# Kernel optimization log

Hardware: AMD Instinct MI355X
Metric: run time of the kernel (lower is better)

The kernel has to match this reference:

```python
import math
import jax, jax.numpy as jnp
import numpy as np

EMBED, HEADS, LEVELS, POINTS = 256, 8, 4, 4
HEAD_DIM = EMBED // HEADS
SHAPES = ((100, 100), (50, 50), (25, 25), (13, 13))  # (h, w) per level
BS, NQ = 8, 900
NV = sum(h * w for h, w in SHAPES)


def _offset_bias():
    # Faithful to init_weights(): per-head rotated grid init for sampling_offsets bias.
    th = np.arange(HEADS, dtype=np.float32) * (2.0 * math.pi / HEADS)
    g = np.stack([np.cos(th), np.sin(th)], -1)
    g = g / np.abs(g).max(-1, keepdims=True)
    g = np.tile(g[:, None, None, :], (1, LEVELS, POINTS, 1))
    g = g * (np.arange(POINTS, dtype=np.float32) + 1.0)[None, None, :, None]
    return jnp.asarray(g.reshape(-1))


def setup_inputs() -> dict:
    key = jax.random.key(0)
    ks = jax.random.split(key, 10)
    s = 0.05
    return {
        "query": jax.random.normal(ks[0], (BS, NQ, EMBED), jnp.float32),
        "value": jax.random.normal(ks[1], (BS, NV, EMBED), jnp.float32),
        "reference_points": jax.random.uniform(ks[2], (BS, NQ, LEVELS, 2), jnp.float32),
        "spatial_shapes": jnp.array(SHAPES, jnp.int32),
        "W_off": jax.random.normal(ks[3], (EMBED, HEADS * LEVELS * POINTS * 2), jnp.float32) * s,
        "b_off": _offset_bias(),
        "W_attn": jax.random.normal(ks[4], (EMBED, HEADS * LEVELS * POINTS), jnp.float32) * s,
        "b_attn": jnp.zeros((HEADS * LEVELS * POINTS,), jnp.float32),
        "W_v": jax.random.normal(ks[5], (EMBED, EMBED), jnp.float32) * s,
        "b_v": jnp.zeros((EMBED,), jnp.float32),
        "W_out": jax.random.normal(ks[6], (EMBED, EMBED), jnp.float32) * s,
        "b_out": jnp.zeros((EMBED,), jnp.float32),
    }


def _bilinear_sample(vl, loc, H, W, aw):
    """grid_sample bilinear, align_corners=False, zero padding, fused with attn weights.

    vl:  (bs, heads, H*W, d)   loc: (bs, nq, heads, P, 2) in [0,1] (x, y)
    aw:  (bs, heads, nq, P)    ->   (bs, heads, nq, d)
    """
    x = loc[..., 0] * W - 0.5
    y = loc[..., 1] * H - 0.5
    x0 = jnp.floor(x)
    y0 = jnp.floor(y)
    lx = x - x0
    ly = y - y0
    x0i = x0.astype(jnp.int32)
    y0i = y0.astype(jnp.int32)
    bs, heads = vl.shape[0], vl.shape[1]
    nq, P = loc.shape[1], loc.shape[3]
    acc = jnp.zeros((bs, heads, nq, vl.shape[-1]), vl.dtype)
    corners = ((0, 0, (1 - lx) * (1 - ly)), (1, 0, lx * (1 - ly)),
               (0, 1, (1 - lx) * ly), (1, 1, lx * ly))
    for dx, dy, wgt in corners:
        xi = x0i + dx
        yi = y0i + dy
        valid = ((xi >= 0) & (xi < W) & (yi >= 0) & (yi < H)).astype(vl.dtype)
        idx = jnp.clip(yi, 0, H - 1) * W + jnp.clip(xi, 0, W - 1)  # (bs, nq, heads, P)
        idx = idx.transpose(0, 2, 1, 3).reshape(bs, heads, nq * P)
        g = jnp.take_along_axis(vl, idx[..., None], axis=2).reshape(bs, heads, nq, P, -1)
        cw = (wgt * valid).transpose(0, 2, 1, 3) * aw  # (bs, heads, nq, P)
        acc = acc + (g * cw[..., None]).sum(3)
    return acc


def reference(query, value, reference_points, spatial_shapes,
              W_off, b_off, W_attn, b_attn, W_v, b_v, W_out, b_out):
    identity = query
    bs, nq, _ = query.shape
    v = (value @ W_v + b_v).reshape(bs, -1, HEADS, HEAD_DIM)
    off = (query @ W_off + b_off).reshape(bs, nq, HEADS, LEVELS, POINTS, 2)
    aw = (query @ W_attn + b_attn).reshape(bs, nq, HEADS, LEVELS * POINTS)
    aw = jax.nn.softmax(aw, -1).reshape(bs, nq, HEADS, LEVELS, POINTS)
    # offset normalizer is (w, h) per level
    norm = jnp.stack([spatial_shapes[:, 1], spatial_shapes[:, 0]], -1).astype(query.dtype)
    loc = reference_points[:, :, None, :, None, :] + off / norm[None, None, None, :, None, :]
    sizes = [h * w for h, w in SHAPES]
    starts = np.cumsum([0] + sizes[:-1])
    out = jnp.zeros((bs, HEADS, nq, HEAD_DIM), query.dtype)
    for l, (h, w) in enumerate(SHAPES):
        vl = jax.lax.dynamic_slice_in_dim(v, int(starts[l]), sizes[l], axis=1)
        vl = vl.transpose(0, 2, 1, 3)  # (bs, heads, h*w, d)
        aw_l = aw[:, :, :, l].transpose(0, 2, 1, 3)  # (bs, heads, nq, P)
        out = out + _bilinear_sample(vl, loc[:, :, :, l], h, w, aw_l)
    out = out.transpose(0, 2, 1, 3).reshape(bs, nq, EMBED)
    return out @ W_out + b_out + identity
```

## Files before the change

### kernel.cpp

```cpp
#include <hip/hip_runtime.h>
#include <hip/hip_bf16.h>

#define EMBED    256
#define HEADS    8
#define LEVELS   4
#define POINTS   4
#define HEAD_DIM 32
#define BS       8
#define NQ       900
#define NV       13294
#define MV       (BS*NV)
#define MQ       (BS*NQ)
#define NQOUT    384

typedef float  f32x4  __attribute__((ext_vector_type(4)));
typedef __bf16 bf16x8 __attribute__((ext_vector_type(8)));
typedef unsigned short ushort8  __attribute__((ext_vector_type(8)));
typedef unsigned short ushort4v __attribute__((ext_vector_type(4)));

__device__ __forceinline__ unsigned short f2bf(float f) {
    unsigned u = __builtin_bit_cast(unsigned, f);
    u += 0x7FFFu + ((u >> 16) & 1u);
    return (unsigned short)(u >> 16);
}
__device__ __forceinline__ float bf2f(unsigned short h) {
    unsigned u = ((unsigned)h) << 16;
    return __builtin_bit_cast(float, u);
}

__global__ __launch_bounds__(256) void prep_kernel(
    const float* __restrict__ Wv,  const float* __restrict__ Woff,
    const float* __restrict__ Wattn, const float* __restrict__ Wout,
    const float* __restrict__ boff, const float* __restrict__ battn,
    unsigned short* __restrict__ WtV, unsigned short* __restrict__ WtQ,
    unsigned short* __restrict__ WtO, float* __restrict__ biasQ)
{
    int n = blockIdx.x;
    int k = threadIdx.x;
    if (n < 256) {
        WtV[n * 256 + k] = f2bf(Wv [k * 256 + n]);
        WtO[n * 256 + k] = f2bf(Wout[k * 256 + n]);
        WtQ[n * 256 + k] = f2bf(Woff[k * 256 + n]);
    } else {
        int j = n - 256;
        WtQ[n * 256 + k] = f2bf(Wattn[k * 128 + j]);
    }
    if (k == 0) biasQ[n] = (n < 256) ? boff[n] : battn[n - 256];
}

template <int WPB, bool OUT_BF16, bool ADD_ID>
struct GemmOps {
    static constexpr int N = WPB * 64;

    __device__ static void load_strip(f32x4 (&pa)[16], const float* __restrict__ A,
                                      int s, int lrow, int kq) {
        const float* ab = A + (size_t)(s * 16 + lrow) * 256 + kq * 8;
        #pragma unroll
        for (int c = 0; c < 8; ++c) {
            pa[2 * c]     = *(const f32x4*)(ab + c * 32);
            pa[2 * c + 1] = *(const f32x4*)(ab + c * 32 + 4);
        }
    }

    __device__ static void compute_store(const f32x4 (&pa)[16],
                                         const bf16x8 (&wf)[4][8],
                                         const f32x4 (&bj)[4],
                                         const float* __restrict__ Ident,
                                         void* __restrict__ Cv,
                                         int s, int lrow, int kq, int n0) {
        f32x4 acc[4];
        #pragma unroll
        for (int j = 0; j < 4; ++j) acc[j] = (f32x4)0.f;
        #pragma unroll
        for (int c = 0; c < 8; ++c) {
            ushort8 vb;
            #pragma unroll
            for (int e = 0; e < 4; ++e) {
                vb[e]     = f2bf(pa[2 * c][e]);
                vb[4 + e] = f2bf(pa[2 * c + 1][e]);
            }
            bf16x8 vf = __builtin_bit_cast(bf16x8, vb);
            #pragma unroll
            for (int j = 0; j < 4; ++j)
                acc[j] = __builtin_amdgcn_mfma_f32_16x16x32_bf16(
                    wf[j][c], vf, acc[j], 0, 0, 0);
        }
        const size_t crow = (size_t)(s * 16 + lrow) * N + n0 + kq * 4;
        #pragma unroll
        for (int j = 0; j < 4; ++j) {
            f32x4 r = acc[j] + bj[j];
            if (ADD_ID)
                r += *(const f32x4*)(Ident + crow + j * 16);
            if (OUT_BF16) {
                ushort4v o;
                #pragma unroll
                for (int e = 0; e < 4; ++e) o[e] = f2bf(r[e]);
                *(ushort4v*)((unsigned short*)Cv + crow + j * 16) = o;
            } else {
                *(f32x4*)((float*)Cv + crow + j * 16) = r;
            }
        }
    }
};

template <int WPB, bool OUT_BF16, bool ADD_ID>
__global__ __launch_bounds__(WPB * 64, 1)
void gemm_regw(const float* __restrict__ A,
               const unsigned short* __restrict__ Bt,
               const float* __restrict__ bias,
               const float* __restrict__ Ident,
               void* __restrict__ Cv, int M)
{
    using Ops = GemmOps<WPB, OUT_BF16, ADD_ID>;
    const int tid  = threadIdx.x;
    const int wave = tid >> 6, lane = tid & 63;
    const int lrow = lane & 15, kq = lane >> 4;
    const int n0   = wave * 64;

    bf16x8 wf[4][8];
    #pragma unroll
    for (int j = 0; j < 4; ++j)
        #pragma unroll
        for (int c = 0; c < 8; ++c)
            wf[j][c] = *(const bf16x8*)(Bt + (size_t)(n0 + j * 16 + lrow) * 256
                                           + c * 32 + kq * 8);
    f32x4 bj[4];
    #pragma unroll
    for (int j = 0; j < 4; ++j)
        bj[j] = *(const f32x4*)(bias + n0 + j * 16 + kq * 4);

    const int NS    = M / 16;
    const int chunk = (NS + gridDim.x - 1) / gridDim.x;
    const int sbeg  = blockIdx.x * chunk;
    const int send  = min(NS, sbeg + chunk);
    if (sbeg >= send) return;

    f32x4 buf0[16], buf1[16];
    Ops::load_strip(buf0, A, sbeg, lrow, kq);
    for (int s = sbeg; s < send; s += 2) {
        if (s + 1 < send) Ops::load_strip(buf1, A, s + 1, lrow, kq);
        Ops::compute_store(buf0, wf, bj, Ident, Cv, s, lrow, kq, n0);
        if (s + 1 < send) {
            if (s + 2 < send) Ops::load_strip(buf0, A, s + 2, lrow, kq);
            Ops::compute_store(buf1, wf, bj, Ident, Cv, s + 1, lrow, kq, n0);
        }
    }
}

__device__ const int   LVL_W[4]  = {100, 50, 25, 13};
__device__ const int   LVL_H[4]  = {100, 50, 25, 13};
__device__ const int   LVL_S[4]  = {0, 10000, 12500, 13125};

__global__ __launch_bounds__(256) void sample_kernel(
    const unsigned short* __restrict__ V,
    const float* __restrict__ Qout,
    const float* __restrict__ RP,
    float* __restrict__ OutS)
{
    const int gid = blockIdx.x * 16 + (threadIdx.x >> 4);
    const int s   = threadIdx.x & 15;
    const int h   = gid & 7;
    const int bq  = gid >> 3;
    const int b   = bq / NQ;

    const float* qrow = Qout + (size_t)bq * NQOUT;

    const int l = s >> 2;
    const float ox = qrow[h * 32 + 2 * s];
    const float oy = qrow[h * 32 + 2 * s + 1];
    float logit    = qrow[256 + h * 16 + s];
    const float rpx = RP[((size_t)bq * 4 + l) * 2 + 0];
    const float rpy = RP[((size_t)bq * 4 + l) * 2 + 1];
    int W = LVL_W[l], H = LVL_H[l], st = LVL_S[l];
    float x = rpx * (float)W + ox - 0.5f;
    float y = rpy * (float)H + oy - 0.5f;
    float fx = floorf(x), fy = floorf(y);
    float lx = x - fx, ly = y - fy;
    int ix = (int)fx, iy = (int)fy;

    float mx = logit;
    #pragma unroll
    for (int o = 8; o; o >>= 1) mx = fmaxf(mx, __shfl_xor(mx, o, 16));
    float e = __expf(logit - mx);
    float sum = e;
    #pragma unroll
    for (int o = 8; o; o >>= 1) sum += __shfl_xor(sum, o, 16);
    const float wgt = e / sum;

    const unsigned short* vb = V + ((size_t)b * NV) * 256 + h * 32 + 2 * s;
    float ax0 = 0.f, ay0 = 0.f, ax1 = 0.f, ay1 = 0.f;

    #pragma unroll
    for (int sp = 0; sp < 16; ++sp) {
        float ws  = __shfl(wgt, sp, 16);
        float lxs = __shfl(lx,  sp, 16);
        float lys = __shfl(ly,  sp, 16);
        int  ixs  = __shfl(ix,  sp, 16);
        int  iys  = __shfl(iy,  sp, 16);
        int  Ws   = __shfl(W,   sp, 16);
        int  Hs   = __shfl(H,   sp, 16);
        int  sts  = __shfl(st,  sp, 16);
        #pragma unroll
        for (int corner = 0; corner < 4; ++corner) {
            int dx = corner & 1, dy = corner >> 1;
            int xi = ixs + dx, yi = iys + dy;
            float valid = (xi >= 0 && xi < Ws && yi >= 0 && yi < Hs) ? 1.f : 0.f;
            int xc = min(max(xi, 0), Ws - 1);
            int yc = min(max(yi, 0), Hs - 1);
            float cw = ws * (dx ? lxs : 1.f - lxs) * (dy ? lys : 1.f - lys) * valid;
            const unsigned short* p = vb + (size_t)(sts + yc * Ws + xc) * 256;
            unsigned pv = *(const unsigned*)p;
            if (corner & 1) {
                ax1 = fmaf(cw, bf2f((unsigned short)(pv & 0xFFFF)), ax1);
                ay1 = fmaf(cw, bf2f((unsigned short)(pv >> 16)), ay1);
            } else {
                ax0 = fmaf(cw, bf2f((unsigned short)(pv & 0xFFFF)), ax0);
                ay0 = fmaf(cw, bf2f((unsigned short)(pv >> 16)), ay0);
            }
        }
    }
    float2* o = (float2*)(OutS + (size_t)bq * 256 + h * 32);
    o[s] = make_float2(ax0 + ax1, ay0 + ay1);
}

extern "C" void kernel_launch(void* const* d_in, const int* in_sizes, int n_in,
                              void* d_out, int out_size, void* d_ws, size_t ws_size,
                              hipStream_t stream)
{
    const float* query  = (const float*)d_in[0];
    const float* value  = (const float*)d_in[1];
    const float* rp     = (const float*)d_in[2];
    const float* W_off  = (const float*)d_in[4];
    const float* b_off  = (const float*)d_in[5];
    const float* W_attn = (const float*)d_in[6];
    const float* b_attn = (const float*)d_in[7];
    const float* W_v    = (const float*)d_in[8];
    const float* b_v    = (const float*)d_in[9];
    const float* W_out  = (const float*)d_in[10];
    const float* b_out  = (const float*)d_in[11];

    char* ws = (char*)d_ws;
    size_t off = 0;
    unsigned short* Vbf = (unsigned short*)(ws + off); off += (size_t)MV * 256 * 2;
    float* qout         = (float*)(ws + off);          off += (size_t)MQ * NQOUT * 4;
    float* outs         = (float*)(ws + off);          off += (size_t)MQ * 256 * 4;
    unsigned short* WtV = (unsigned short*)(ws + off); off += 256 * 256 * 2;
    unsigned short* WtQ = (unsigned short*)(ws + off); off += 384 * 256 * 2;
    unsigned short* WtO = (unsigned short*)(ws + off); off += 256 * 256 * 2;
    float* biasQ        = (float*)(ws + off);          off += 384 * 4;

    prep_kernel<<<384, 256, 0, stream>>>(W_v, W_off, W_attn, W_out, b_off, b_attn,
                                         WtV, WtQ, WtO, biasQ);

    gemm_regw<4, true, false><<<512, 256, 0, stream>>>(
        value, WtV, b_v, nullptr, Vbf, MV);

    gemm_regw<6, false, false><<<450, 384, 0, stream>>>(
        query, WtQ, biasQ, nullptr, qout, MQ);

    sample_kernel<<<(BS * NQ * HEADS) / 16, 256, 0, stream>>>(Vbf, qout, rp, outs);

    gemm_regw<4, false, true><<<450, 256, 0, stream>>>(
        outs, WtO, b_out, query, (float*)d_out, MQ);
}
```

Baseline: 317.6 us.

## Stage GEMM weights in LDS and split N across grid blocks

Replaces the register-resident-weight GEMM with a version that copies a 128-column weight slice into padded shared memory and reads MFMA B fragments from LDS. The N dimension is split across blockIdx.y, and two waves per column set take alternating row strips, with A loaded in half-K pieces to overlap loads with compute. This is meant to lower register pressure so more waves fit per CU, at the cost of extra LDS reads, re-reading A once per N slice, and launch_bounds no longer capping occupancy at 1.

Result: faster. 285.3 us (-10.2%).

```diff
diff --git a/kernel.cpp b/kernel.cpp
--- a/kernel.cpp
+++ b/kernel.cpp
@@ -49,43 +49,85 @@
 }
 
 template <int WPB, bool OUT_BF16, bool ADD_ID>
-struct GemmOps {
-    static constexpr int N = WPB * 64;
-
-    __device__ static void load_strip(f32x4 (&pa)[16], const float* __restrict__ A,
-                                      int s, int lrow, int kq) {
-        const float* ab = A + (size_t)(s * 16 + lrow) * 256 + kq * 8;
-        #pragma unroll
-        for (int c = 0; c < 8; ++c) {
-            pa[2 * c]     = *(const f32x4*)(ab + c * 32);
-            pa[2 * c + 1] = *(const f32x4*)(ab + c * 32 + 4);
-        }
-    }
-
-    __device__ static void compute_store(const f32x4 (&pa)[16],
-                                         const bf16x8 (&wf)[4][8],
-                                         const f32x4 (&bj)[4],
-                                         const float* __restrict__ Ident,
-                                         void* __restrict__ Cv,
-                                         int s, int lrow, int kq, int n0) {
-        f32x4 acc[4];
-        #pragma unroll
-        for (int j = 0; j < 4; ++j) acc[j] = (f32x4)0.f;
-        #pragma unroll
-        for (int c = 0; c < 8; ++c) {
+__global__ __launch_bounds__(WPB * 128)
+void gemm_ldsw(const float* __restrict__ A,
+               const unsigned short* __restrict__ Bt,
+               const float* __restrict__ bias,
+               const float* __restrict__ Ident,
+               void* __restrict__ Cv, int M, int Ntot)
+{
+    constexpr int NC   = WPB * 64;
+    constexpr int NTHR = WPB * 128;
+    const int n0g = blockIdx.y * NC;
+    __shared__ unsigned short Ws[NC * 272];
+
+    const int tid = threadIdx.x;
+    #pragma unroll
+    for (int i = 0; i < (NC * 256 / 8) / NTHR; ++i) {
+        int flat = i * NTHR + tid;
+        int row = flat >> 5, col = (flat & 31) * 8;
+        *(ushort8*)&Ws[row * 272 + col] =
+            *(const ushort8*)(Bt + (size_t)(n0g + row) * 256 + col);
+    }
+    __syncthreads();
+
+    const int wave = tid >> 6, lane = tid & 63;
+    const int colset = wave % WPB, parity = wave / WPB;
+    const int lrow = lane & 15, kq = lane >> 4;
+    const int n0 = colset * 64;
+
+    f32x4 bj[4];
+    #pragma unroll
+    for (int j = 0; j < 4; ++j)
+        bj[j] = *(const f32x4*)(bias + n0g + n0 + j * 16 + kq * 4);
+
+    const int NS    = M / 16;
+    const int chunk = (NS + gridDim.x - 1) / gridDim.x;
+    const int send  = min(NS, blockIdx.x * chunk + chunk);
+    int s = blockIdx.x * chunk + parity;
+    if (s >= send) return;
+
+    auto loadHalf = [&](f32x4 (&b)[8], int ss, int h) {
+        const float* ab = A + (size_t)(ss * 16 + lrow) * 256 + h * 128 + kq * 8;
+        #pragma unroll
+        for (int c = 0; c < 4; ++c) {
+            b[2 * c]     = *(const f32x4*)(ab + c * 32);
+            b[2 * c + 1] = *(const f32x4*)(ab + c * 32 + 4);
+        }
+    };
+    auto computeHalf = [&](f32x4 (&b)[8], int h, f32x4 (&acc)[4]) {
+        #pragma unroll
+        for (int c = 0; c < 4; ++c) {
             ushort8 vb;
             #pragma unroll
             for (int e = 0; e < 4; ++e) {
-                vb[e]     = f2bf(pa[2 * c][e]);
-                vb[4 + e] = f2bf(pa[2 * c + 1][e]);
+                vb[e]     = f2bf(b[2 * c][e]);
+                vb[4 + e] = f2bf(b[2 * c + 1][e]);
             }
             bf16x8 vf = __builtin_bit_cast(bf16x8, vb);
             #pragma unroll
-            for (int j = 0; j < 4; ++j)
-                acc[j] = __builtin_amdgcn_mfma_f32_16x16x32_bf16(
-                    wf[j][c], vf, acc[j], 0, 0, 0);
-        }
-        const size_t crow = (size_t)(s * 16 + lrow) * N + n0 + kq * 4;
+            for (int j = 0; j < 4; ++j) {
+                bf16x8 wf = *(const bf16x8*)
+                    &Ws[(n0 + j * 16 + lrow) * 272 + h * 128 + c * 32 + kq * 8];
+                acc[j] = __builtin_amdgcn_mfma_f32_16x16x32_bf16(wf, vf, acc[j], 0, 0, 0);
+            }
+        }
+    };
+
+    f32x4 b0[8], b1[8];
+    loadHalf(b0, s, 0);
+    while (true) {
+        loadHalf(b1, s, 1);
+        f32x4 acc[4];
+        #pragma unroll
+        for (int j = 0; j < 4; ++j) acc[j] = (f32x4)0.f;
+        computeHalf(b0, 0, acc);
+        const int sn = s + 2;
+        const bool more = sn < send;
+        if (more) loadHalf(b0, sn, 0);
+        computeHalf(b1, 1, acc);
+
+        const size_t crow = (size_t)(s * 16 + lrow) * Ntot + n0g + n0 + kq * 4;
         #pragma unroll
         for (int j = 0; j < 4; ++j) {
             f32x4 r = acc[j] + bj[j];
@@ -100,50 +142,8 @@
                 *(f32x4*)((float*)Cv + crow + j * 16) = r;
             }
         }
-    }
-};
-
-template <int WPB, bool OUT_BF16, bool ADD_ID>
-__global__ __launch_bounds__(WPB * 64, 1)
-void gemm_regw(const float* __restrict__ A,
-               const unsigned short* __restrict__ Bt,
-               const float* __restrict__ bias,
-               const float* __restrict__ Ident,
-               void* __restrict__ Cv, int M)
-{
-    using Ops = GemmOps<WPB, OUT_BF16, ADD_ID>;
-    const int tid  = threadIdx.x;
-    const int wave = tid >> 6, lane = tid & 63;
-    const int lrow = lane & 15, kq = lane >> 4;
-    const int n0   = wave * 64;
-
-    bf16x8 wf[4][8];
-    #pragma unroll
-    for (int j = 0; j < 4; ++j)
-        #pragma unroll
-        for (int c = 0; c < 8; ++c)
-            wf[j][c] = *(const bf16x8*)(Bt + (size_t)(n0 + j * 16 + lrow) * 256
-                                           + c * 32 + kq * 8);
-    f32x4 bj[4];
-    #pragma unroll
-    for (int j = 0; j < 4; ++j)
-        bj[j] = *(const f32x4*)(bias + n0 + j * 16 + kq * 4);
-
-    const int NS    = M / 16;
-    const int chunk = (NS + gridDim.x - 1) / gridDim.x;
-    const int sbeg  = blockIdx.x * chunk;
-    const int send  = min(NS, sbeg + chunk);
-    if (sbeg >= send) return;
-
-    f32x4 buf0[16], buf1[16];
-    Ops::load_strip(buf0, A, sbeg, lrow, kq);
-    for (int s = sbeg; s < send; s += 2) {
-        if (s + 1 < send) Ops::load_strip(buf1, A, s + 1, lrow, kq);
-        Ops::compute_store(buf0, wf, bj, Ident, Cv, s, lrow, kq, n0);
-        if (s + 1 < send) {
-            if (s + 2 < send) Ops::load_strip(buf0, A, s + 2, lrow, kq);
-            Ops::compute_store(buf1, wf, bj, Ident, Cv, s + 1, lrow, kq, n0);
-        }
+        if (!more) break;
+        s = sn;
     }
 }
 
@@ -252,14 +252,14 @@
     prep_kernel<<<384, 256, 0, stream>>>(W_v, W_off, W_attn, W_out, b_off, b_attn,
                                          WtV, WtQ, WtO, biasQ);
 
-    gemm_regw<4, true, false><<<512, 256, 0, stream>>>(
-        value, WtV, b_v, nullptr, Vbf, MV);
-
-    gemm_regw<6, false, false><<<450, 384, 0, stream>>>(
-        query, WtQ, biasQ, nullptr, qout, MQ);
+    gemm_ldsw<2, true, false><<<dim3(256, 2), 256, 0, stream>>>(
+        value, WtV, b_v, nullptr, Vbf, MV, 256);
+
+    gemm_ldsw<2, false, false><<<dim3(225, 3), 256, 0, stream>>>(
+        query, WtQ, biasQ, nullptr, qout, MQ, NQOUT);
 
     sample_kernel<<<(BS * NQ * HEADS) / 16, 256, 0, stream>>>(Vbf, qout, rp, outs);
 
-    gemm_regw<4, false, true><<<450, 256, 0, stream>>>(
-        outs, WtO, b_out, query, (float*)d_out, MQ);
-}
+    gemm_ldsw<2, false, true><<<dim3(225, 2), 256, 0, stream>>>(
+        outs, WtO, b_out, query, (float*)d_out, MQ, 256);
+}
```
